# Performance work log

Hardware: AMD Instinct MI355X
Metric: run time of the kernel (lower is better)

## Reference

```python
import jax, jax.numpy as jnp
import numpy as np

B, T, SC, D, N, K, H = 2, 1024, 1024, 2048, 16, 4, 128
SOFTCAP = 50.0
BIG_NEG = -2.3819763e38


def _apply_rope(x, positions, max_wavelength=10_000):
    # x: [B, T, heads, H], positions: [B, T]
    h = x.shape[-1]
    freq_exponents = (2.0 / h) * jnp.arange(h // 2, dtype=jnp.float32)
    timescale = max_wavelength ** freq_exponents
    radians = positions[..., None].astype(jnp.float32) / timescale  # [B,T,H/2]
    radians = radians[..., None, :]  # [B,T,1,H/2]
    sin, cos = jnp.sin(radians), jnp.cos(radians)
    x1, x2 = jnp.split(x, 2, axis=-1)
    out = jnp.concatenate([x1 * cos - x2 * sin, x2 * cos + x1 * sin], axis=-1)
    return out.astype(x.dtype)


def setup_inputs() -> dict:
    key = jax.random.key(0)
    ks = jax.random.split(key, 6)
    x = jax.random.normal(ks[0], (B, T, D), jnp.float32)
    # new-token positions follow the cache: SC .. SC+T-1
    positions = jnp.broadcast_to(SC + jnp.arange(T, dtype=jnp.int32), (B, T))
    # causal mask over concatenated [cache | new] keys
    q_pos = SC + jnp.arange(T)
    k_pos = jnp.arange(SC + T)
    attn_mask = jnp.broadcast_to(
        (k_pos[None, :] <= q_pos[:, None])[None, None], (B, 1, T, SC + T)
    )
    cache_k = jax.random.normal(ks[1], (B, SC, K, H), jnp.float32)
    cache_v = jax.random.normal(ks[2], (B, SC, K, H), jnp.float32)
    wq = jax.random.normal(ks[3], (N, D, H), jnp.float32) * (D ** -0.5)
    wkv = jax.random.normal(ks[4], (2, K, D, H), jnp.float32) * (D ** -0.5)
    wout = jax.random.normal(ks[5], (N, H, D), jnp.float32) * ((N * H) ** -0.5)
    return {"x": x, "positions": positions, "attn_mask": attn_mask,
            "cache_k": cache_k, "cache_v": cache_v,
            "wq": wq, "wkv": wkv, "wout": wout}


def reference(x, positions, attn_mask, cache_k, cache_v, wq, wkv, wout):
    dtype = x.dtype
    h = wq.shape[-1]
    k_heads = wkv.shape[1]
    # projections (GQA path: separate q and fused kv einsums)
    q = jnp.einsum('BTD,NDH->BTNH', x, wq.astype(dtype))
    kv = jnp.einsum('BSD,cKDH->cBSKH', x, wkv.astype(dtype))
    k, v = kv[0], kv[1]
    # RoPE then query pre-attn scaling (rsqrt_head_dim)
    q = _apply_rope(q, positions) * (h ** -0.5)
    k = _apply_rope(k, positions)
    # KV cache concat along sequence axis
    k = jnp.concatenate([cache_k.astype(dtype), k], axis=1)
    v = jnp.concatenate([cache_v.astype(dtype), v], axis=1)
    b, t, n, _ = q.shape
    g = n // k_heads
    q = q.reshape(b, t, k_heads, g, h)  # B T K G H
    logits = jnp.einsum('BTKGH,BSKH->BKGTS', q, k,
                        preferred_element_type=jnp.float32)
    # tanh logits softcap
    logits = jnp.tanh(logits / SOFTCAP) * SOFTCAP
    masked = jnp.where(attn_mask[:, :, None, :, :], logits, BIG_NEG)
    probs = jax.nn.softmax(masked, axis=-1).astype(dtype)
    encoded = jnp.einsum('BKGTS,BSKH->BTKGH', probs, v)
    encoded = encoded.reshape(b, t, n, h)
    out = jnp.einsum('BTNH,NHD->BTD', encoded, wout.astype(dtype))
    return out
```

## Files before the change

### kernel.cpp

```cpp
#include <hip/hip_runtime.h>
#include <stdint.h>
#include <stddef.h>


typedef __bf16 bf16_t;
typedef __bf16 bf16x8 __attribute__((ext_vector_type(8)));
typedef __bf16 bf16x4 __attribute__((ext_vector_type(4)));
typedef float  f32x4  __attribute__((ext_vector_type(4)));

#define GLDS16(gsrc, ldst)                                                      \
  __builtin_amdgcn_global_load_lds(                                             \
      (const __attribute__((address_space(1))) void*)(gsrc),                    \
      (__attribute__((address_space(3))) void*)(ldst), 16, 0, 0)

__global__ __launch_bounds__(256)
void k_prep(const float* __restrict__ x, bf16_t* __restrict__ xb,
            const float* __restrict__ wq, const float* __restrict__ wkv,
            const float* __restrict__ wout,
            bf16_t* __restrict__ w1t, bf16_t* __restrict__ wot) {
  __shared__ bf16_t tile[64][65];
  const int blk = blockIdx.x;
  const int tid = threadIdx.x;
  if (blk < 4096) {
    int i = blk * 256 + tid;
    f32x4 v = *(const f32x4*)(x + (size_t)i * 4);
    bf16x4 o;
    o[0] = (bf16_t)v[0]; o[1] = (bf16_t)v[1]; o[2] = (bf16_t)v[2]; o[3] = (bf16_t)v[3];
    *(bf16x4*)(xb + (size_t)i * 4) = o;
    return;
  }
  const float* s; bf16_t* d; int R, C, bx, by;
  if (blk < 5120) {
    int local = blk - 4096;
    int z = local >> 6, rem = local & 63;
    by = rem >> 1; bx = rem & 1;
    R = 2048; C = 128;
    s = wq + (size_t)z * 2048 * 128;
    d = w1t + (size_t)z * 128 * 2048;
  } else if (blk < 5632) {
    int local = blk - 5120;
    int z = local >> 6, rem = local & 63;
    by = rem >> 1; bx = rem & 1;
    R = 2048; C = 128;
    s = wkv + (size_t)z * 2048 * 128;
    d = w1t + (size_t)2048 * 2048 + (size_t)z * 128 * 2048;
  } else {
    int local = blk - 5632;
    bx = local & 31; by = local >> 5;
    R = 2048; C = 2048;
    s = wout; d = wot;
  }
  const int c0 = bx * 64, r0 = by * 64;
#pragma unroll
  for (int it = 0; it < 16; ++it) {
    int idx = it * 256 + tid;
    int rl = idx >> 6, cl = idx & 63;
    tile[rl][cl] = (bf16_t)s[(size_t)(r0 + rl) * C + (c0 + cl)];
  }
  __syncthreads();
#pragma unroll
  for (int it = 0; it < 16; ++it) {
    int idx = it * 256 + tid;
    int cl = idx >> 6, rl = idx & 63;
    d[(size_t)(c0 + cl) * R + (r0 + rl)] = tile[rl][cl];
  }
}

__global__ __launch_bounds__(512)
void k_gemm_bt(const bf16_t* __restrict__ A, const bf16_t* __restrict__ Bt,
               float* __restrict__ C, int M, int N, int Kd) {
  __shared__ char gsm[65536];
  const int tid = threadIdx.x;
  const int w = tid >> 6, l = tid & 63;
  const int wq = w & 3, wr = wq >> 1, wc = wq & 1, wk = w >> 2;
  const int lr = l & 15, lk = l >> 4;
  const int nwg = gridDim.x * gridDim.y;
  const int bid = blockIdx.y * gridDim.x + blockIdx.x;
  const int cpx = nwg >> 3;
  const int sid = (bid & 7) * cpx + (bid >> 3);
  const int row0 = (sid % gridDim.x) * 128;
  const int col0 = (sid / gridDim.x) * 128;

  auto stage = [&](int buf, int k0) {
#pragma unroll
    for (int inst = 0; inst < 2; ++inst) {
      uint32_t oo = (uint32_t)(inst * 8192 + tid * 16);
      uint32_t r  = oo >> 7;
      uint32_t kb = (oo ^ (((oo >> 7) & 7u) << 4)) & 127u;
      GLDS16((const char*)(A + (size_t)(row0 + r) * Kd + k0) + kb,
             gsm + buf * 16384 + oo);
      GLDS16((const char*)(Bt + (size_t)(col0 + r) * Kd + k0) + kb,
             gsm + 32768 + buf * 16384 + oo);
    }
  };

  f32x4 acc[4][4] = {};
  stage(0, 0);
  asm volatile("s_waitcnt vmcnt(0)" ::: "memory");
  __builtin_amdgcn_s_barrier();
  int cur = 0;
  for (int k0 = 0; k0 < Kd; k0 += 64) {
    const int kn = (k0 + 64 < Kd) ? (k0 + 64) : k0;
    stage(cur ^ 1, kn);
    const char* Ab = gsm + cur * 16384;
    const char* Bb = gsm + 32768 + cur * 16384;
    bf16x8 af[4], bfr[4];
#pragma unroll
    for (int m = 0; m < 4; ++m) {
      uint32_t r = (uint32_t)(wr * 64 + m * 16 + lr);
      uint32_t a = (r * 128u + (uint32_t)(wk * 64 + lk * 16)) ^ ((r & 7u) << 4);
      af[m] = *(const bf16x8*)(Ab + a);
    }
#pragma unroll
    for (int n = 0; n < 4; ++n) {
      uint32_t r = (uint32_t)(wc * 64 + n * 16 + lr);
      uint32_t a = (r * 128u + (uint32_t)(wk * 64 + lk * 16)) ^ ((r & 7u) << 4);
      bfr[n] = *(const bf16x8*)(Bb + a);
    }
    __builtin_amdgcn_s_setprio(1);
#pragma unroll
    for (int m = 0; m < 4; ++m)
#pragma unroll
      for (int n = 0; n < 4; ++n)
        acc[m][n] = __builtin_amdgcn_mfma_f32_16x16x32_bf16(af[m], bfr[n], acc[m][n], 0, 0, 0);
    __builtin_amdgcn_s_setprio(0);
    asm volatile("s_waitcnt vmcnt(0)" ::: "memory");
    __builtin_amdgcn_s_barrier();
    __builtin_amdgcn_sched_barrier(0);
    cur ^= 1;
  }
  if (wk == 1) {
#pragma unroll
    for (int m = 0; m < 4; ++m)
#pragma unroll
      for (int n = 0; n < 4; ++n)
        *(f32x4*)(gsm + wq * 16384 + ((m * 4 + n) * 64 + l) * 16) = acc[m][n];
  }
  __syncthreads();
  if (wk == 0) {
#pragma unroll
    for (int m = 0; m < 4; ++m) {
      const int rr = row0 + wr * 64 + m * 16 + lk * 4;
#pragma unroll
      for (int n = 0; n < 4; ++n) {
        f32x4 o = *(const f32x4*)(gsm + wq * 16384 + ((m * 4 + n) * 64 + l) * 16);
        const int cc = col0 + wc * 64 + n * 16 + lr;
        float* cp = C + (size_t)rr * N + cc;
#pragma unroll
        for (int j = 0; j < 4; ++j) cp[(size_t)j * N] = acc[m][n][j] + o[j];
      }
    }
  }
}

__global__ __launch_bounds__(256)
void k_pre2(const float* __restrict__ qkv, const int* __restrict__ positions,
            const float* __restrict__ ck, const float* __restrict__ cv,
            bf16_t* __restrict__ Qr, bf16_t* __restrict__ Kf, bf16_t* __restrict__ Vt) {
  __shared__ char shm[16512];
  const int blk = blockIdx.x;
  const int tid = threadIdx.x;
  if (blk < 2048) {
    const int row = blk;
    const int b = row >> 10, t = row & 1023;
    float* cs = (float*)shm;
    float* sn = (float*)shm + 64;
    if (tid < 64) {
      float fe = (float)tid * (2.0f / 128.0f);
      float rad = (float)positions[row] * __builtin_amdgcn_exp2f(-fe * 13.287712379549449f);
      sn[tid] = __sinf(rad);
      cs[tid] = __cosf(rad);
    }
    __syncthreads();
    const float* rowp = qkv + (size_t)row * 3072;
    const float qs = 0.08838834764831845f;
#pragma unroll
    for (int it = 0; it < 8; ++it) {
      int idx = it * 256 + tid;
      int n = idx >> 7, hh = idx & 127;
      int hp = hh & 63;
      float x1 = rowp[n * 128 + hp];
      float x2 = rowp[n * 128 + 64 + hp];
      float o = (hh < 64) ? (x1 * cs[hp] - x2 * sn[hp]) : (x2 * cs[hp] + x1 * sn[hp]);
      Qr[(((size_t)b * 16 + n) * 1024 + t) * 128 + hh] = (bf16_t)(o * qs);
    }
#pragma unroll
    for (int it = 0; it < 2; ++it) {
      int idx = it * 256 + tid;
      int kh = idx >> 7, hh = idx & 127;
      int hp = hh & 63;
      float x1 = rowp[2048 + kh * 128 + hp];
      float x2 = rowp[2048 + kh * 128 + 64 + hp];
      float o = (hh < 64) ? (x1 * cs[hp] - x2 * sn[hp]) : (x2 * cs[hp] + x1 * sn[hp]);
      Kf[(((size_t)b * 4 + kh) * 2048 + 1024 + t) * 128 + hh] = (bf16_t)o;
    }
    return;
  }
  if (blk < 4096) {
    const int row = blk - 2048;
    const int b = row >> 10, s = row & 1023;
    const float* src = ck + (size_t)row * 512;
#pragma unroll
    for (int it = 0; it < 2; ++it) {
      int idx = it * 256 + tid;
      int kh = idx >> 7, hh = idx & 127;
      Kf[(((size_t)b * 4 + kh) * 2048 + s) * 128 + hh] = (bf16_t)src[idx];
    }
    return;
  }
  {
    const int local = blk - 4096;
    const int s0 = (local & 31) * 64;
    const int bk = local >> 5;
    const int b = bk >> 2, kh = bk & 3;
    bf16_t (*vt)[129] = (bf16_t(*)[129])shm;
#pragma unroll
    for (int it = 0; it < 32; ++it) {
      int idx = it * 256 + tid;
      int sl = idx >> 7, hh = idx & 127;
      int s = s0 + sl;
      float v = (s < 1024)
        ? cv[(((size_t)b * 1024 + s) * 4 + kh) * 128 + hh]
        : qkv[((size_t)b * 1024 + (s - 1024)) * 3072 + 2560 + kh * 128 + hh];
      vt[sl][hh] = (bf16_t)v;
    }
    __syncthreads();
#pragma unroll
    for (int it = 0; it < 32; ++it) {
      int idx = it * 256 + tid;
      int hh = idx >> 6, sl = idx & 63;
      Vt[((size_t)bk * 128 + hh) * 2048 + s0 + sl] = vt[sl][hh];
    }
  }
}

__global__ __launch_bounds__(512)
void k_attn(const bf16_t* __restrict__ Qr, const bf16_t* __restrict__ Kf,
            const bf16_t* __restrict__ Vt, bf16_t* __restrict__ enc) {
  __shared__ char smem[74240];
  const int bid = blockIdx.y * gridDim.x + blockIdx.x;
  const int sid = (bid & 7) * 64 + (bid >> 3);
  const int qsel = sid & 15;
  const int bn = sid >> 4;
  const int qblk = ((bn >> 1) & 1) ? (15 - qsel) : qsel;
  const int b = bn >> 4, n = bn & 15;
  const int kh = n >> 2;
  const int tid = threadIdx.x;
  const int w = tid >> 6, l = tid & 63;
  const int qg = w & 1, sw = w >> 1;
  const int window = sw >> 1, hg = sw & 1;
  const int lr = l & 15, lk = l >> 4;
  const bf16_t* Kbase = Kf + ((size_t)b * 4 + kh) * 2048 * 128;
  const bf16_t* Vbase = Vt + ((size_t)b * 4 + kh) * 128 * 2048;
  float* psL = (float*)(smem + 73728);

  bf16x8 aq[2][4];
#pragma unroll
  for (int qf = 0; qf < 2; ++qf) {
    const bf16_t* qp = Qr + ((size_t)bn * 1024 + qblk * 64 + qg * 32 + qf * 16 + lr) * 128;
#pragma unroll
    for (int kk = 0; kk < 4; ++kk) aq[qf][kk] = *(const bf16x8*)(qp + kk * 32 + lk * 8);
  }

  auto stageK = [&](int buf, int s0) {
#pragma unroll
    for (int inst = 0; inst < 2; ++inst) {
      uint32_t oo = (uint32_t)(inst * 8192 + tid * 16);
      uint32_t r  = oo >> 8;
      uint32_t kb = (oo ^ (((oo >> 8) & 7u) << 4)) & 255u;
      GLDS16((const char*)(Kbase + (size_t)(s0 + r) * 128) + kb,
             smem + buf * 16384 + oo);
    }
  };
  auto stageV = [&](int buf, int s0) {
#pragma unroll
    for (int inst = 0; inst < 2; ++inst) {
      uint32_t oo = (uint32_t)(inst * 8192 + tid * 16);
      uint32_t r  = oo >> 7;
      uint32_t sb = (oo ^ (((oo >> 7) & 7u) << 4)) & 127u;
      GLDS16((const char*)(Vbase + (size_t)r * 2048 + s0) + sb,
             smem + 32768 + buf * 16384 + oo);
    }
  };

  char* Pq = smem + 65536 + qg * 4096;
  f32x4 acc[2][4] = {};
  float psum[2] = {0.f, 0.f};
  const int ntiles = 17 + qblk;
  const int qglob0 = 1024 + qblk * 64 + qg * 32 + lr;

  if (tid < 64) psL[tid] = 0.f;
  stageK(0, 0);
  stageV(0, 0);
  asm volatile("s_waitcnt vmcnt(0)" ::: "memory");
  __builtin_amdgcn_s_barrier();
  int cur = 0;

  for (int st = 0; st < ntiles; ++st) {
    const int s0 = st * 64;
    const int sn = (st + 1 < ntiles) ? (s0 + 64) : s0;
    stageK(cur ^ 1, sn);
    stageV(cur ^ 1, sn);
    const char* Kc = smem + cur * 16384;
    const char* Vc = smem + 32768 + cur * 16384;

    f32x4 sacc[2] = {};
    __builtin_amdgcn_s_setprio(1);
#pragma unroll
    for (int kk = 0; kk < 4; ++kk) {
      uint32_t r = (uint32_t)(sw * 16 + lr);
      uint32_t a = (r * 256u + (uint32_t)(kk * 64 + lk * 16)) ^ ((r & 7u) << 4);
      bf16x8 ak = *(const bf16x8*)(Kc + a);
      sacc[0] = __builtin_amdgcn_mfma_f32_16x16x32_bf16(ak, aq[0][kk], sacc[0], 0, 0, 0);
      sacc[1] = __builtin_amdgcn_mfma_f32_16x16x32_bf16(ak, aq[1][kk], sacc[1], 0, 0, 0);
    }
    __builtin_amdgcn_s_setprio(0);

    const bool last = (st == ntiles - 1);
#pragma unroll
    for (int qf = 0; qf < 2; ++qf) {
      const int q = qf * 16 + lr;
      bf16x4 pq;
#pragma unroll
      for (int j = 0; j < 4; ++j) {
        float lg = sacc[qf][j];
        float t  = lg * 1.4426950408889634f;
        float u  = 1.0f - (lg * lg) * (1.0f / 7500.0f);
        float p  = __builtin_amdgcn_exp2f(t * u);
        if (last) {
          int sg = s0 + sw * 16 + lk * 4 + j;
          if (sg > qglob0 + qf * 16) p = 0.0f;
        }
        psum[qf] += p;
        pq[j] = (bf16_t)p;
      }
      uint32_t a = ((uint32_t)(q * 128) + (uint32_t)(sw * 32 + lk * 8)) ^ (((uint32_t)lr & 7u) << 4);
      *(bf16x4*)(Pq + a) = pq;
    }
    asm volatile("s_waitcnt lgkmcnt(0)" ::: "memory");
    __builtin_amdgcn_s_barrier();
    __builtin_amdgcn_sched_barrier(0);

    {
      bf16x8 pa[2];
#pragma unroll
      for (int qf = 0; qf < 2; ++qf) {
        uint32_t a = ((uint32_t)((qf * 16 + lr) * 128) + (uint32_t)(window * 64 + lk * 16)) ^ (((uint32_t)lr & 7u) << 4);
        pa[qf] = *(const bf16x8*)(Pq + a);
      }
      __builtin_amdgcn_s_setprio(1);
#pragma unroll
      for (int i = 0; i < 4; ++i) {
        uint32_t h = (uint32_t)((hg * 4 + i) * 16 + lr);
        uint32_t va = (h * 128u + (uint32_t)(window * 64 + lk * 16)) ^ ((h & 7u) << 4);
        bf16x8 bv = *(const bf16x8*)(Vc + va);
        acc[0][i] = __builtin_amdgcn_mfma_f32_16x16x32_bf16(pa[0], bv, acc[0][i], 0, 0, 0);
        acc[1][i] = __builtin_amdgcn_mfma_f32_16x16x32_bf16(pa[1], bv, acc[1][i], 0, 0, 0);
      }
      __builtin_amdgcn_s_setprio(0);
    }
    asm volatile("s_waitcnt vmcnt(0)" ::: "memory");
    __builtin_amdgcn_s_barrier();
    __builtin_amdgcn_sched_barrier(0);
    cur ^= 1;
  }

  float ps0 = psum[0];
  ps0 += __shfl_xor(ps0, 16); ps0 += __shfl_xor(ps0, 32);
  float ps1 = psum[1];
  ps1 += __shfl_xor(ps1, 16); ps1 += __shfl_xor(ps1, 32);
  if (l < 16) {
    atomicAdd(&psL[qg * 32 + lr], ps0);
    atomicAdd(&psL[qg * 32 + 16 + lr], ps1);
  }
  float* accL = (float*)smem;
  if (window == 1) {
    char* sb = (char*)(accL) + (qg * 2 + hg) * 8192;
#pragma unroll
    for (int qf = 0; qf < 2; ++qf)
#pragma unroll
      for (int i = 0; i < 4; ++i) {
        uint32_t a = (uint32_t)(l * 128) + ((uint32_t)((qf * 4 + i) * 16) ^ (((uint32_t)l & 7u) << 4));
        *(f32x4*)(sb + a) = acc[qf][i];
      }
  }
  __syncthreads();
  if (window == 0) {
    char* sb = (char*)(accL) + (qg * 2 + hg) * 8192;
    float inv[2][4];
#pragma unroll
    for (int qf = 0; qf < 2; ++qf)
#pragma unroll
      for (int j = 0; j < 4; ++j)
        inv[qf][j] = 1.0f / (psL[qg * 32 + qf * 16 + lk * 4 + j] + 1e-30f);
#pragma unroll
    for (int qf = 0; qf < 2; ++qf) {
#pragma unroll
      for (int i = 0; i < 4; ++i) {
        uint32_t a = (uint32_t)(l * 128) + ((uint32_t)((qf * 4 + i) * 16) ^ (((uint32_t)l & 7u) << 4));
        f32x4 o2 = *(const f32x4*)(sb + a);
        const int col = n * 128 + (hg * 4 + i) * 16 + lr;
#pragma unroll
        for (int j = 0; j < 4; ++j) {
          int trow = qblk * 64 + qg * 32 + qf * 16 + lk * 4 + j;
          enc[((size_t)b * 1024 + trow) * 2048 + col] =
              (bf16_t)((acc[qf][i][j] + o2[j]) * inv[qf][j]);
        }
      }
    }
  }
}

extern "C" void kernel_launch(void* const* d_in, const int* in_sizes, int n_in,
                              void* d_out, int out_size, void* d_ws, size_t ws_size,
                              hipStream_t stream) {
  (void)in_sizes; (void)n_in; (void)out_size; (void)ws_size;
  const float* x    = (const float*)d_in[0];
  const int*   pos  = (const int*)d_in[1];
  const float* ck   = (const float*)d_in[3];
  const float* cv   = (const float*)d_in[4];
  const float* wq   = (const float*)d_in[5];
  const float* wkv  = (const float*)d_in[6];
  const float* wout = (const float*)d_in[7];
  float* out = (float*)d_out;

  char* p = (char*)d_ws;
  bf16_t* xb  = (bf16_t*)p; p += (size_t)2048 * 2048 * 2;
  bf16_t* w1t = (bf16_t*)p; p += (size_t)3072 * 2048 * 2;
  float*  qkv = (float*) p; p += (size_t)2048 * 3072 * 4;
  bf16_t* Qr  = (bf16_t*)p; p += (size_t)32 * 1024 * 128 * 2;
  bf16_t* Kf  = (bf16_t*)p; p += (size_t)8 * 2048 * 128 * 2;
  bf16_t* Vt  = (bf16_t*)p; p += (size_t)8 * 128 * 2048 * 2;
  bf16_t* enc = (bf16_t*)p; p += (size_t)2048 * 2048 * 2;
  bf16_t* wot = (bf16_t*)p; p += (size_t)2048 * 2048 * 2;

  k_prep<<<6656, 256, 0, stream>>>(x, xb, wq, wkv, wout, w1t, wot);
  k_gemm_bt<<<dim3(16, 24), 512, 0, stream>>>(xb, w1t, qkv, 2048, 3072, 2048);
  k_pre2<<<4352, 256, 0, stream>>>(qkv, pos, ck, cv, Qr, Kf, Vt);
  k_attn<<<dim3(16, 32), 512, 0, stream>>>(Qr, Kf, Vt, enc);
  k_gemm_bt<<<dim3(16, 16), 512, 0, stream>>>(enc, wot, out, 2048, 2048, 2048);
}
```

Baseline: 132.9 us.

## Fuse RoPE, scaling and K/V layout writes into QKV GEMM epilogue

The QKV projection GEMM now applies RoPE and query scaling in its epilogue and writes bf16 Q, K and transposed V directly into the attention layouts. This removes the fp32 qkv intermediate round-trip and the separate k_pre2 launch. Cache K/V conversion moves into the prep kernel. The epilogue recomputes sin/cos per element and does strided per-element bf16 stores, which may be less efficient than the old separate pass.

```diff
diff --git a/kernel.cpp b/kernel.cpp
--- a/kernel.cpp
+++ b/kernel.cpp
@@ -17,8 +17,10 @@
 void k_prep(const float* __restrict__ x, bf16_t* __restrict__ xb,
             const float* __restrict__ wq, const float* __restrict__ wkv,
             const float* __restrict__ wout,
-            bf16_t* __restrict__ w1t, bf16_t* __restrict__ wot) {
-  __shared__ bf16_t tile[64][65];
+            bf16_t* __restrict__ w1t, bf16_t* __restrict__ wot,
+            const float* __restrict__ ck, const float* __restrict__ cv,
+            bf16_t* __restrict__ Kf, bf16_t* __restrict__ Vt) {
+  __shared__ char shm[16512];
   const int blk = blockIdx.x;
   const int tid = threadIdx.x;
   if (blk < 4096) {
@@ -29,40 +31,215 @@
     *(bf16x4*)(xb + (size_t)i * 4) = o;
     return;
   }
-  const float* s; bf16_t* d; int R, C, bx, by;
-  if (blk < 5120) {
-    int local = blk - 4096;
-    int z = local >> 6, rem = local & 63;
-    by = rem >> 1; bx = rem & 1;
-    R = 2048; C = 128;
-    s = wq + (size_t)z * 2048 * 128;
-    d = w1t + (size_t)z * 128 * 2048;
-  } else if (blk < 5632) {
-    int local = blk - 5120;
-    int z = local >> 6, rem = local & 63;
-    by = rem >> 1; bx = rem & 1;
-    R = 2048; C = 128;
-    s = wkv + (size_t)z * 2048 * 128;
-    d = w1t + (size_t)2048 * 2048 + (size_t)z * 128 * 2048;
+  if (blk < 6656) {
+    const float* s; bf16_t* d; int R, C, bx, by;
+    if (blk < 5120) {
+      int local = blk - 4096;
+      int z = local >> 6, rem = local & 63;
+      by = rem >> 1; bx = rem & 1;
+      R = 2048; C = 128;
+      s = wq + (size_t)z * 2048 * 128;
+      d = w1t + (size_t)z * 128 * 2048;
+    } else if (blk < 5632) {
+      int local = blk - 5120;
+      int z = local >> 6, rem = local & 63;
+      by = rem >> 1; bx = rem & 1;
+      R = 2048; C = 128;
+      s = wkv + (size_t)z * 2048 * 128;
+      d = w1t + (size_t)2048 * 2048 + (size_t)z * 128 * 2048;
+    } else {
+      int local = blk - 5632;
+      bx = local & 31; by = local >> 5;
+      R = 2048; C = 2048;
+      s = wout; d = wot;
+    }
+    bf16_t (*tile)[65] = (bf16_t(*)[65])shm;
+    const int c0 = bx * 64, r0 = by * 64;
+#pragma unroll
+    for (int it = 0; it < 16; ++it) {
+      int idx = it * 256 + tid;
+      int rl = idx >> 6, cl = idx & 63;
+      tile[rl][cl] = (bf16_t)s[(size_t)(r0 + rl) * C + (c0 + cl)];
+    }
+    __syncthreads();
+#pragma unroll
+    for (int it = 0; it < 16; ++it) {
+      int idx = it * 256 + tid;
+      int cl = idx >> 6, rl = idx & 63;
+      d[(size_t)(c0 + cl) * R + (r0 + rl)] = tile[rl][cl];
+    }
+    return;
+  }
+  if (blk < 8704) {
+    const int row = blk - 6656;
+    const int b = row >> 10, s = row & 1023;
+    const float* src = ck + (size_t)row * 512;
+#pragma unroll
+    for (int it = 0; it < 2; ++it) {
+      int idx = it * 256 + tid;
+      int kh = idx >> 7, hh = idx & 127;
+      Kf[(((size_t)b * 4 + kh) * 2048 + s) * 128 + hh] = (bf16_t)src[idx];
+    }
+    return;
+  }
+  {
+    const int local = blk - 8704;
+    const int s0 = (local & 15) * 64;
+    const int bk = local >> 4;
+    const int b = bk >> 2, kh = bk & 3;
+    bf16_t (*vt)[129] = (bf16_t(*)[129])shm;
+#pragma unroll
+    for (int it = 0; it < 32; ++it) {
+      int idx = it * 256 + tid;
+      int sl = idx >> 7, hh = idx & 127;
+      vt[sl][hh] = (bf16_t)cv[(((size_t)b * 1024 + s0 + sl) * 4 + kh) * 128 + hh];
+    }
+    __syncthreads();
+#pragma unroll
+    for (int it = 0; it < 32; ++it) {
+      int idx = it * 256 + tid;
+      int hh = idx >> 6, sl = idx & 63;
+      Vt[((size_t)bk * 128 + hh) * 2048 + s0 + sl] = vt[sl][hh];
+    }
+  }
+}
+
+__global__ __launch_bounds__(512)
+void k_gemm_qkv(const bf16_t* __restrict__ A, const bf16_t* __restrict__ Bt,
+                const int* __restrict__ positions,
+                bf16_t* __restrict__ Qr, bf16_t* __restrict__ Kf,
+                bf16_t* __restrict__ Vt) {
+  __shared__ char gsm[65536];
+  const int tid = threadIdx.x;
+  const int w = tid >> 6, l = tid & 63;
+  const int wq = w & 3, wr = wq >> 1, wc = wq & 1, wk = w >> 2;
+  const int lr = l & 15, lk = l >> 4;
+  const int nwg = gridDim.x * gridDim.y;
+  const int bid = blockIdx.y * gridDim.x + blockIdx.x;
+  const int cpx = nwg >> 3;
+  const int sid = (bid & 7) * cpx + (bid >> 3);
+  const int row0 = (sid % gridDim.x) * 128;
+  const int col0 = (sid / gridDim.x) * 128;
+
+  auto stage = [&](int buf, int k0) {
+#pragma unroll
+    for (int inst = 0; inst < 2; ++inst) {
+      uint32_t oo = (uint32_t)(inst * 8192 + tid * 16);
+      uint32_t r  = oo >> 7;
+      uint32_t kb = (oo ^ (((oo >> 7) & 7u) << 4)) & 127u;
+      GLDS16((const char*)(A + (size_t)(row0 + r) * 2048 + k0) + kb,
+             gsm + buf * 16384 + oo);
+      GLDS16((const char*)(Bt + (size_t)(col0 + r) * 2048 + k0) + kb,
+             gsm + 32768 + buf * 16384 + oo);
+    }
+  };
+
+  f32x4 acc[4][4] = {};
+  stage(0, 0);
+  asm volatile("s_waitcnt vmcnt(0)" ::: "memory");
+  __builtin_amdgcn_s_barrier();
+  int cur = 0;
+  for (int k0 = 0; k0 < 2048; k0 += 64) {
+    const int kn = (k0 + 64 < 2048) ? (k0 + 64) : k0;
+    stage(cur ^ 1, kn);
+    const char* Ab = gsm + cur * 16384;
+    const char* Bb = gsm + 32768 + cur * 16384;
+    bf16x8 af[4], bfr[4];
+#pragma unroll
+    for (int m = 0; m < 4; ++m) {
+      uint32_t r = (uint32_t)(wr * 64 + m * 16 + lr);
+      uint32_t a = (r * 128u + (uint32_t)(wk * 64 + lk * 16)) ^ ((r & 7u) << 4);
+      af[m] = *(const bf16x8*)(Ab + a);
+    }
+#pragma unroll
+    for (int n = 0; n < 4; ++n) {
+      uint32_t r = (uint32_t)(wc * 64 + n * 16 + lr);
+      uint32_t a = (r * 128u + (uint32_t)(wk * 64 + lk * 16)) ^ ((r & 7u) << 4);
+      bfr[n] = *(const bf16x8*)(Bb + a);
+    }
+    __builtin_amdgcn_s_setprio(1);
+#pragma unroll
+    for (int m = 0; m < 4; ++m)
+#pragma unroll
+      for (int n = 0; n < 4; ++n)
+        acc[m][n] = __builtin_amdgcn_mfma_f32_16x16x32_bf16(af[m], bfr[n], acc[m][n], 0, 0, 0);
+    __builtin_amdgcn_s_setprio(0);
+    asm volatile("s_waitcnt vmcnt(0)" ::: "memory");
+    __builtin_amdgcn_s_barrier();
+    __builtin_amdgcn_sched_barrier(0);
+    cur ^= 1;
+  }
+
+  if (wk == 1) {
+#pragma unroll
+    for (int m = 0; m < 4; ++m)
+#pragma unroll
+      for (int n = 0; n < 4; ++n)
+        *(f32x4*)(gsm + wq * 16384 + ((m * 4 + n) * 64 + l) * 16) = acc[m][n];
+  }
+  __syncthreads();
+  if (wk == 0) {
+#pragma unroll
+    for (int m = 0; m < 4; ++m)
+#pragma unroll
+      for (int n = 0; n < 4; ++n) {
+        f32x4 o = *(const f32x4*)(gsm + wq * 16384 + ((m * 4 + n) * 64 + l) * 16);
+        f32x4 s = acc[m][n];
+        s[0] += o[0]; s[1] += o[1]; s[2] += o[2]; s[3] += o[3];
+        *(f32x4*)(gsm + wq * 16384 + ((m * 4 + n) * 64 + l) * 16) = s;
+      }
+  }
+  __syncthreads();
+
+  const int hb = col0 >> 7;
+  const int bb = row0 >> 10;
+  const int tb = row0 & 1023;
+  const int h  = tid & 127;
+  const int tq0 = (tid >> 7) * 8;
+
+  auto cslot = [&](int t, int hc) -> const f32x4* {
+    int wrt = t >> 6, mt = (t >> 4) & 3, lkt = (t >> 2) & 3;
+    int wch = hc >> 6, nh = (hc >> 4) & 3, lrh = hc & 15;
+    return (const f32x4*)(gsm + (wrt * 2 + wch) * 16384 +
+                          (((mt * 4 + nh) * 64 + lkt * 16 + lrh) << 4));
+  };
+
+  if (hb < 20) {
+    const int hp = h & 63;
+    const bool hi = h >= 64;
+    const float invts = __builtin_amdgcn_exp2f(-(float)hp * (13.287712379549449f / 64.0f));
+    const float qs = 0.08838834764831845f;
+    bf16_t* basep;
+    float scale;
+    if (hb < 16) { basep = Qr + (((size_t)bb * 16 + hb) * 1024 + tb) * 128 + h; scale = qs; }
+    else         { basep = Kf + (((size_t)bb * 4 + (hb - 16)) * 2048 + 1024 + tb) * 128 + h; scale = 1.0f; }
+#pragma unroll
+    for (int iq = 0; iq < 8; ++iq) {
+      const int tq = tq0 + iq;
+      f32x4 c1 = *cslot(tq * 4, hp);
+      f32x4 c2 = *cslot(tq * 4, hp + 64);
+#pragma unroll
+      for (int j = 0; j < 4; ++j) {
+        const int tl = tq * 4 + j;
+        float rad = (float)positions[row0 + tl] * invts;
+        float sv = __sinf(rad), cvv = __cosf(rad);
+        float o = hi ? (c2[j] * cvv + c1[j] * sv) : (c1[j] * cvv - c2[j] * sv);
+        basep[(size_t)tl * 128] = (bf16_t)(o * scale);
+      }
+    }
   } else {
-    int local = blk - 5632;
-    bx = local & 31; by = local >> 5;
-    R = 2048; C = 2048;
-    s = wout; d = wot;
-  }
-  const int c0 = bx * 64, r0 = by * 64;
-#pragma unroll
-  for (int it = 0; it < 16; ++it) {
-    int idx = it * 256 + tid;
-    int rl = idx >> 6, cl = idx & 63;
-    tile[rl][cl] = (bf16_t)s[(size_t)(r0 + rl) * C + (c0 + cl)];
-  }
-  __syncthreads();
-#pragma unroll
-  for (int it = 0; it < 16; ++it) {
-    int idx = it * 256 + tid;
-    int cl = idx >> 6, rl = idx & 63;
-    d[(size_t)(c0 + cl) * R + (r0 + rl)] = tile[rl][cl];
+    const int kh = hb - 20;
+    bf16_t vbuf[32];
+#pragma unroll
+    for (int iq = 0; iq < 8; ++iq) {
+      f32x4 c1 = *cslot((tq0 + iq) * 4, h);
+#pragma unroll
+      for (int j = 0; j < 4; ++j) vbuf[iq * 4 + j] = (bf16_t)c1[j];
+    }
+    bf16_t* vp = Vt + (((size_t)bb * 4 + kh) * 128 + h) * 2048 + 1024 + tb + tq0 * 4;
+#pragma unroll
+    for (int c4 = 0; c4 < 4; ++c4)
+      *(bf16x8*)(vp + c4 * 8) = *(const bf16x8*)&vbuf[c4 * 8];
   }
 }
 
@@ -149,87 +326,6 @@
 #pragma unroll
         for (int j = 0; j < 4; ++j) cp[(size_t)j * N] = acc[m][n][j] + o[j];
       }
-    }
-  }
-}
-
-__global__ __launch_bounds__(256)
-void k_pre2(const float* __restrict__ qkv, const int* __restrict__ positions,
-            const float* __restrict__ ck, const float* __restrict__ cv,
-            bf16_t* __restrict__ Qr, bf16_t* __restrict__ Kf, bf16_t* __restrict__ Vt) {
-  __shared__ char shm[16512];
-  const int blk = blockIdx.x;
-  const int tid = threadIdx.x;
-  if (blk < 2048) {
-    const int row = blk;
-    const int b = row >> 10, t = row & 1023;
-    float* cs = (float*)shm;
-    float* sn = (float*)shm + 64;
-    if (tid < 64) {
-      float fe = (float)tid * (2.0f / 128.0f);
-      float rad = (float)positions[row] * __builtin_amdgcn_exp2f(-fe * 13.287712379549449f);
-      sn[tid] = __sinf(rad);
-      cs[tid] = __cosf(rad);
-    }
-    __syncthreads();
-    const float* rowp = qkv + (size_t)row * 3072;
-    const float qs = 0.08838834764831845f;
-#pragma unroll
-    for (int it = 0; it < 8; ++it) {
-      int idx = it * 256 + tid;
-      int n = idx >> 7, hh = idx & 127;
-      int hp = hh & 63;
-      float x1 = rowp[n * 128 + hp];
-      float x2 = rowp[n * 128 + 64 + hp];
-      float o = (hh < 64) ? (x1 * cs[hp] - x2 * sn[hp]) : (x2 * cs[hp] + x1 * sn[hp]);
-      Qr[(((size_t)b * 16 + n) * 1024 + t) * 128 + hh] = (bf16_t)(o * qs);
-    }
-#pragma unroll
-    for (int it = 0; it < 2; ++it) {
-      int idx = it * 256 + tid;
-      int kh = idx >> 7, hh = idx & 127;
-      int hp = hh & 63;
-      float x1 = rowp[2048 + kh * 128 + hp];
-      float x2 = rowp[2048 + kh * 128 + 64 + hp];
-      float o = (hh < 64) ? (x1 * cs[hp] - x2 * sn[hp]) : (x2 * cs[hp] + x1 * sn[hp]);
-      Kf[(((size_t)b * 4 + kh) * 2048 + 1024 + t) * 128 + hh] = (bf16_t)o;
-    }
-    return;
-  }
-  if (blk < 4096) {
-    const int row = blk - 2048;
-    const int b = row >> 10, s = row & 1023;
-    const float* src = ck + (size_t)row * 512;
-#pragma unroll
-    for (int it = 0; it < 2; ++it) {
-      int idx = it * 256 + tid;
-      int kh = idx >> 7, hh = idx & 127;
-      Kf[(((size_t)b * 4 + kh) * 2048 + s) * 128 + hh] = (bf16_t)src[idx];
-    }
-    return;
-  }
-  {
-    const int local = blk - 4096;
-    const int s0 = (local & 31) * 64;
-    const int bk = local >> 5;
-    const int b = bk >> 2, kh = bk & 3;
-    bf16_t (*vt)[129] = (bf16_t(*)[129])shm;
-#pragma unroll
-    for (int it = 0; it < 32; ++it) {
-      int idx = it * 256 + tid;
-      int sl = idx >> 7, hh = idx & 127;
-      int s = s0 + sl;
-      float v = (s < 1024)
-        ? cv[(((size_t)b * 1024 + s) * 4 + kh) * 128 + hh]
-        : qkv[((size_t)b * 1024 + (s - 1024)) * 3072 + 2560 + kh * 128 + hh];
-      vt[sl][hh] = (bf16_t)v;
-    }
-    __syncthreads();
-#pragma unroll
-    for (int it = 0; it < 32; ++it) {
-      int idx = it * 256 + tid;
-      int hh = idx >> 6, sl = idx & 63;
-      Vt[((size_t)bk * 128 + hh) * 2048 + s0 + sl] = vt[sl][hh];
     }
   }
 }
@@ -427,16 +523,14 @@
   char* p = (char*)d_ws;
   bf16_t* xb  = (bf16_t*)p; p += (size_t)2048 * 2048 * 2;
   bf16_t* w1t = (bf16_t*)p; p += (size_t)3072 * 2048 * 2;
-  float*  qkv = (float*) p; p += (size_t)2048 * 3072 * 4;
   bf16_t* Qr  = (bf16_t*)p; p += (size_t)32 * 1024 * 128 * 2;
   bf16_t* Kf  = (bf16_t*)p; p += (size_t)8 * 2048 * 128 * 2;
   bf16_t* Vt  = (bf16_t*)p; p += (size_t)8 * 128 * 2048 * 2;
   bf16_t* enc = (bf16_t*)p; p += (size_t)2048 * 2048 * 2;
   bf16_t* wot = (bf16_t*)p; p += (size_t)2048 * 2048 * 2;
 
-  k_prep<<<6656, 256, 0, stream>>>(x, xb, wq, wkv, wout, w1t, wot);
-  k_gemm_bt<<<dim3(16, 24), 512, 0, stream>>>(xb, w1t, qkv, 2048, 3072, 2048);
-  k_pre2<<<4352, 256, 0, stream>>>(qkv, pos, ck, cv, Qr, Kf, Vt);
+  k_prep<<<8832, 256, 0, stream>>>(x, xb, wq, wkv, wout, w1t, wot, ck, cv, Kf, Vt);
+  k_gemm_qkv<<<dim3(16, 24), 512, 0, stream>>>(xb, w1t, pos, Qr, Kf, Vt);
   k_attn<<<dim3(16, 32), 512, 0, stream>>>(Qr, Kf, Vt, enc);
   k_gemm_bt<<<dim3(16, 16), 512, 0, stream>>>(enc, wot, out, 2048, 2048, 2048);
 }
```

Result: slower. 143.6 us (+8.0%).
